# Kernel tuning notes

Hardware: AMD Instinct MI355X
Metric: run time of the kernel (lower is better)

## Reference

```python
import jax, jax.numpy as jnp
import numpy as np

INPUT, HIDDEN, CLASSES = 28, 128, 10

def setup_inputs() -> dict:
    key = jax.random.key(0)
    ks = jax.random.split(key, 8)
    B = 16384
    s_ih = 1.0 / np.sqrt(HIDDEN)
    return {
        "x": jax.random.normal(ks[0], (B, 1, 28, 28), dtype=jnp.float32),
        "W_ih": jax.random.uniform(ks[1], (HIDDEN, INPUT), jnp.float32, -s_ih, s_ih),
        "W_hh": jax.random.uniform(ks[2], (HIDDEN, HIDDEN), jnp.float32, -s_ih, s_ih),
        "b_ih": jax.random.uniform(ks[3], (HIDDEN,), jnp.float32, -s_ih, s_ih),
        "b_hh": jax.random.uniform(ks[4], (HIDDEN,), jnp.float32, -s_ih, s_ih),
        "W_fc": jax.random.uniform(ks[5], (CLASSES, HIDDEN), jnp.float32, -s_ih, s_ih),
        "b_fc": jax.random.uniform(ks[6], (CLASSES,), jnp.float32, -s_ih, s_ih),
    }

def reference(x, W_ih, W_hh, b_ih, b_hh, W_fc, b_fc):
    # x: [B,1,28,28] -> squeeze channel -> [B,T=28,I=28]
    xs = jnp.squeeze(x, axis=1)
    B = xs.shape[0]
    # precompute input projections for all timesteps: [B,T,H]
    xproj = jnp.einsum("bti,hi->bth", xs, W_ih) + b_ih + b_hh
    xproj_t = jnp.transpose(xproj, (1, 0, 2))  # [T,B,H]

    def step(h, xp):
        h_new = jnp.tanh(xp + h @ W_hh.T)
        return h_new, None

    h0 = jnp.zeros((B, HIDDEN), dtype=xs.dtype)
    h_last, _ = jax.lax.scan(step, h0, xproj_t)
    return h_last @ W_fc.T + b_fc  # [B, num_classes]
```

## Files before the change

### kernel.cpp

```cpp
#include <hip/hip_runtime.h>
#include <hip/hip_bf16.h>
#include <stdint.h>


typedef __attribute__((ext_vector_type(8))) short short8;
typedef __attribute__((ext_vector_type(4))) float f32x4;

union Frag { short8 s; uint32_t u[4]; };

#define MFMA16(a,b,c) __builtin_amdgcn_mfma_f32_16x16x32_bf16((a),(b),(c),0,0,0)

__device__ __forceinline__ uint32_t pk2(float a, float b){
    union { __hip_bfloat162 h; uint32_t u; } cv;
    cv.h = __float22bfloat162_rn(make_float2(a,b));
    return cv.u;
}
__device__ __forceinline__ float lo16f(uint32_t u){ return __builtin_bit_cast(float, u<<16); }
__device__ __forceinline__ float hi16f(uint32_t u){ return __builtin_bit_cast(float, u & 0xffff0000u); }

__device__ __forceinline__ void cvt8(const f32x4& a, const f32x4& b, Frag& hi, Frag& lo){
    float v[8];
    #pragma unroll
    for(int i=0;i<4;i++){ v[i]=a[i]; v[4+i]=b[i]; }
    #pragma unroll
    for(int q=0;q<4;q++){
        uint32_t h = pk2(v[2*q], v[2*q+1]);
        hi.u[q] = h;
        lo.u[q] = pk2(v[2*q]-lo16f(h), v[2*q+1]-hi16f(h));
    }
}

__device__ __forceinline__ int piperm(int p){
    int jt = p>>4, c = p&15;
    return 32*(jt>>1) + 8*(c>>2) + 4*(jt&1) + (c&3);
}

__device__ __forceinline__ float fast_tanh(float x){
    x = fminf(fmaxf(x, -30.f), 30.f);
    float e = __expf(2.f*x);
    return (e-1.f)*__builtin_amdgcn_rcpf(e+1.f);
}

__global__ __launch_bounds__(64,1) void rnn_fused(
    const float* __restrict__ x,   const float* __restrict__ Wih,
    const float* __restrict__ Whh, const float* __restrict__ bih,
    const float* __restrict__ bhh, const float* __restrict__ Wfc,
    const float* __restrict__ bfc, float* __restrict__ out)
{
    const int lane = threadIdx.x & 63;
    const int g = lane>>4, c = lane&15;
    const int b0 = blockIdx.x*16;
    const f32x4 zero4 = {0.f,0.f,0.f,0.f};

    Frag whh_h[8][4], whh_l[8][4];
    #pragma unroll
    for(int jt=0;jt<8;jt++){
        const int row = piperm(16*jt + c);
        const float* rp = Whh + row*128;
        #pragma unroll
        for(int kt=0;kt<4;kt++){
            f32x4 a = *(const f32x4*)(rp + kt*32 + 8*g);
            f32x4 b = *(const f32x4*)(rp + kt*32 + 8*g + 4);
            cvt8(a, b, whh_h[jt][kt], whh_l[jt][kt]);
        }
    }

    Frag wih_h[8], wih_l[8];
    {
        const int i1 = 8*g;
        const int i2 = (g<3) ? (8*g+4) : 24;
        #pragma unroll
        for(int jt=0;jt<8;jt++){
            const int row = piperm(16*jt + c);
            const float* rp = Wih + row*28;
            f32x4 a = *(const f32x4*)(rp + i1);
            f32x4 b = *(const f32x4*)(rp + i2);
            if (g==3) b = zero4;
            cvt8(a, b, wih_h[jt], wih_l[jt]);
        }
    }

    f32x4 biasr[8];
    #pragma unroll
    for(int jt=0;jt<8;jt++){
        #pragma unroll
        for(int r=0;r<4;r++){
            int q = piperm(16*jt + 4*g + r);
            biasr[jt][r] = bih[q] + bhh[q];
        }
    }

    Frag bh_h[4], bh_l[4];
    #pragma unroll
    for(int kt=0;kt<4;kt++){
        #pragma unroll
        for(int q=0;q<4;q++){ bh_h[kt].u[q]=0; bh_l[kt].u[q]=0; }
    }

    const float* xrow = x + (size_t)(b0 + c)*784;
    const int o1 = 8*g;
    const int o2 = (g<3) ? (8*g+4) : 24;

    f32x4 xA = *(const f32x4*)(xrow + o1);
    f32x4 xB = *(const f32x4*)(xrow + o2);

    for(int t=0; t<28; ++t){
        f32x4 xA_n = xA, xB_n = xB;
        if (t < 27){
            xA_n = *(const f32x4*)(xrow + (t+1)*28 + o1);
            xB_n = *(const f32x4*)(xrow + (t+1)*28 + o2);
        }
        Frag bx_h, bx_l;
        {
            f32x4 b = xB;
            if (g==3) b = zero4;
            cvt8(xA, b, bx_h, bx_l);
        }
        f32x4 acc[8];
        #pragma unroll
        for(int jt=0;jt<8;jt++){
            acc[jt] = MFMA16(wih_h[jt].s, bx_h.s, biasr[jt]);
            acc[jt] = MFMA16(wih_l[jt].s, bx_h.s, acc[jt]);
            acc[jt] = MFMA16(wih_h[jt].s, bx_l.s, acc[jt]);
            #pragma unroll
            for(int kt=0;kt<4;kt++){
                acc[jt] = MFMA16(whh_h[jt][kt].s, bh_h[kt].s, acc[jt]);
                acc[jt] = MFMA16(whh_l[jt][kt].s, bh_h[kt].s, acc[jt]);
                acc[jt] = MFMA16(whh_h[jt][kt].s, bh_l[kt].s, acc[jt]);
            }
        }
        Frag nh_h[4], nh_l[4];
        #pragma unroll
        for(int jt=0;jt<8;jt++){
            float h0 = fast_tanh(acc[jt][0]);
            float h1 = fast_tanh(acc[jt][1]);
            float h2 = fast_tanh(acc[jt][2]);
            float h3 = fast_tanh(acc[jt][3]);
            const int kt = jt>>1, q0 = (jt&1)*2;
            uint32_t u0 = pk2(h0,h1), u1 = pk2(h2,h3);
            nh_h[kt].u[q0]   = u0;
            nh_h[kt].u[q0+1] = u1;
            nh_l[kt].u[q0]   = pk2(h0-lo16f(u0), h1-hi16f(u0));
            nh_l[kt].u[q0+1] = pk2(h2-lo16f(u1), h3-hi16f(u1));
        }
        #pragma unroll
        for(int kt=0;kt<4;kt++){ bh_h[kt]=nh_h[kt]; bh_l[kt]=nh_l[kt]; }
        xA = xA_n; xB = xB_n;
    }

    Frag wfc_h[4], wfc_l[4];
    {
        const bool valid = (c < 10);
        const float* rp = Wfc + (valid ? c : 0)*128;
        #pragma unroll
        for(int kt=0;kt<4;kt++){
            f32x4 a = *(const f32x4*)(rp + kt*32 + 8*g);
            f32x4 b = *(const f32x4*)(rp + kt*32 + 8*g + 4);
            if(!valid){ a = zero4; b = zero4; }
            cvt8(a, b, wfc_h[kt], wfc_l[kt]);
        }
    }
    f32x4 accf = {0.f,0.f,0.f,0.f};
    #pragma unroll
    for(int kt=0;kt<4;kt++){
        accf = MFMA16(wfc_h[kt].s, bh_h[kt].s, accf);
        accf = MFMA16(wfc_l[kt].s, bh_h[kt].s, accf);
        accf = MFMA16(wfc_h[kt].s, bh_l[kt].s, accf);
    }
    #pragma unroll
    for(int r=0;r<4;r++){
        int cls = 4*g + r;
        if (cls < 10){
            out[(size_t)(b0+c)*10 + cls] = accf[r] + bfc[cls];
        }
    }
}

extern "C" void kernel_launch(void* const* d_in, const int* in_sizes, int n_in,
                              void* d_out, int out_size, void* d_ws, size_t ws_size,
                              hipStream_t stream)
{
    const float* x   = (const float*)d_in[0];
    const float* Wih = (const float*)d_in[1];
    const float* Whh = (const float*)d_in[2];
    const float* bih = (const float*)d_in[3];
    const float* bhh = (const float*)d_in[4];
    const float* Wfc = (const float*)d_in[5];
    const float* bfc = (const float*)d_in[6];
    float* out = (float*)d_out;

    const int nb = in_sizes[0] / 784;
    dim3 grid(nb/16), blk(64);
    hipLaunchKernelGGL(rnn_fused, grid, blk, 0, stream,
                       x, Wih, Whh, bih, bhh, Wfc, bfc, out);
}
```

Before: 163.6 us.

## Split hidden units across four waves with LDS exchange of hidden state

Each block now uses four wavefronts instead of one. Each wave owns two of the eight hidden-row tiles and keeps only its share of W_hh/W_ih in registers. The new hidden state is exchanged every timestep through double-buffered shared memory and a block barrier. The MFMA chain is also split into two independent accumulators to shorten the dependency chain. This cuts per-wave register pressure and serial MFMA latency per step, at the cost of a __syncthreads and LDS traffic on every timestep.

```diff
diff --git a/kernel.cpp b/kernel.cpp
--- a/kernel.cpp
+++ b/kernel.cpp
@@ -5,8 +5,9 @@
 
 typedef __attribute__((ext_vector_type(8))) short short8;
 typedef __attribute__((ext_vector_type(4))) float f32x4;
-
-union Frag { short8 s; uint32_t u[4]; };
+typedef __attribute__((ext_vector_type(4))) uint32_t u32x4;
+
+union Frag { short8 s; uint32_t u[4]; u32x4 v; };
 
 #define MFMA16(a,b,c) __builtin_amdgcn_mfma_f32_16x16x32_bf16((a),(b),(c),0,0,0)
 
@@ -41,52 +42,56 @@
     return (e-1.f)*__builtin_amdgcn_rcpf(e+1.f);
 }
 
-__global__ __launch_bounds__(64,1) void rnn_fused(
+__global__ __launch_bounds__(256,2) void rnn_fused4(
     const float* __restrict__ x,   const float* __restrict__ Wih,
     const float* __restrict__ Whh, const float* __restrict__ bih,
     const float* __restrict__ bhh, const float* __restrict__ Wfc,
     const float* __restrict__ bfc, float* __restrict__ out)
 {
-    const int lane = threadIdx.x & 63;
+    const int tid  = threadIdx.x;
+    const int w    = tid >> 6;
+    const int lane = tid & 63;
     const int g = lane>>4, c = lane&15;
     const int b0 = blockIdx.x*16;
     const f32x4 zero4 = {0.f,0.f,0.f,0.f};
 
-    Frag whh_h[8][4], whh_l[8][4];
-    #pragma unroll
-    for(int jt=0;jt<8;jt++){
-        const int row = piperm(16*jt + c);
+    __shared__ uint32_t lds[2][2][4][64][4];
+
+    Frag whh_h[2][4], whh_l[2][4];
+    #pragma unroll
+    for(int j=0;j<2;j++){
+        const int row = piperm(16*(2*w+j) + c);
         const float* rp = Whh + row*128;
         #pragma unroll
         for(int kt=0;kt<4;kt++){
             f32x4 a = *(const f32x4*)(rp + kt*32 + 8*g);
             f32x4 b = *(const f32x4*)(rp + kt*32 + 8*g + 4);
-            cvt8(a, b, whh_h[jt][kt], whh_l[jt][kt]);
-        }
-    }
-
-    Frag wih_h[8], wih_l[8];
+            cvt8(a, b, whh_h[j][kt], whh_l[j][kt]);
+        }
+    }
+
+    Frag wih_h[2], wih_l[2];
     {
         const int i1 = 8*g;
         const int i2 = (g<3) ? (8*g+4) : 24;
         #pragma unroll
-        for(int jt=0;jt<8;jt++){
-            const int row = piperm(16*jt + c);
+        for(int j=0;j<2;j++){
+            const int row = piperm(16*(2*w+j) + c);
             const float* rp = Wih + row*28;
             f32x4 a = *(const f32x4*)(rp + i1);
             f32x4 b = *(const f32x4*)(rp + i2);
             if (g==3) b = zero4;
-            cvt8(a, b, wih_h[jt], wih_l[jt]);
-        }
-    }
-
-    f32x4 biasr[8];
-    #pragma unroll
-    for(int jt=0;jt<8;jt++){
+            cvt8(a, b, wih_h[j], wih_l[j]);
+        }
+    }
+
+    f32x4 biasr[2];
+    #pragma unroll
+    for(int j=0;j<2;j++){
         #pragma unroll
         for(int r=0;r<4;r++){
-            int q = piperm(16*jt + 4*g + r);
-            biasr[jt][r] = bih[q] + bhh[q];
+            int q = piperm(16*(2*w+j) + 4*g + r);
+            biasr[j][r] = bih[q] + bhh[q];
         }
     }
 
@@ -116,40 +121,54 @@
             if (g==3) b = zero4;
             cvt8(xA, b, bx_h, bx_l);
         }
-        f32x4 acc[8];
-        #pragma unroll
-        for(int jt=0;jt<8;jt++){
-            acc[jt] = MFMA16(wih_h[jt].s, bx_h.s, biasr[jt]);
-            acc[jt] = MFMA16(wih_l[jt].s, bx_h.s, acc[jt]);
-            acc[jt] = MFMA16(wih_h[jt].s, bx_l.s, acc[jt]);
-            #pragma unroll
-            for(int kt=0;kt<4;kt++){
-                acc[jt] = MFMA16(whh_h[jt][kt].s, bh_h[kt].s, acc[jt]);
-                acc[jt] = MFMA16(whh_l[jt][kt].s, bh_h[kt].s, acc[jt]);
-                acc[jt] = MFMA16(whh_h[jt][kt].s, bh_l[kt].s, acc[jt]);
-            }
-        }
-        Frag nh_h[4], nh_l[4];
-        #pragma unroll
-        for(int jt=0;jt<8;jt++){
-            float h0 = fast_tanh(acc[jt][0]);
-            float h1 = fast_tanh(acc[jt][1]);
-            float h2 = fast_tanh(acc[jt][2]);
-            float h3 = fast_tanh(acc[jt][3]);
-            const int kt = jt>>1, q0 = (jt&1)*2;
+        f32x4 acc[2];
+        #pragma unroll
+        for(int j=0;j<2;j++){
+            f32x4 a1 = MFMA16(wih_h[j].s, bx_h.s, biasr[j]);
+            a1 = MFMA16(wih_l[j].s, bx_h.s, a1);
+            a1 = MFMA16(wih_h[j].s, bx_l.s, a1);
+            a1 = MFMA16(whh_h[j][0].s, bh_h[0].s, a1);
+            a1 = MFMA16(whh_l[j][0].s, bh_h[0].s, a1);
+            a1 = MFMA16(whh_h[j][0].s, bh_l[0].s, a1);
+            a1 = MFMA16(whh_h[j][1].s, bh_h[1].s, a1);
+            a1 = MFMA16(whh_l[j][1].s, bh_h[1].s, a1);
+            a1 = MFMA16(whh_h[j][1].s, bh_l[1].s, a1);
+            f32x4 a2 = MFMA16(whh_h[j][2].s, bh_h[2].s, zero4);
+            a2 = MFMA16(whh_l[j][2].s, bh_h[2].s, a2);
+            a2 = MFMA16(whh_h[j][2].s, bh_l[2].s, a2);
+            a2 = MFMA16(whh_h[j][3].s, bh_h[3].s, a2);
+            a2 = MFMA16(whh_l[j][3].s, bh_h[3].s, a2);
+            a2 = MFMA16(whh_h[j][3].s, bh_l[3].s, a2);
+            acc[j] = a1 + a2;
+        }
+        Frag nh_h, nh_l;
+        #pragma unroll
+        for(int j=0;j<2;j++){
+            float h0 = fast_tanh(acc[j][0]);
+            float h1 = fast_tanh(acc[j][1]);
+            float h2 = fast_tanh(acc[j][2]);
+            float h3 = fast_tanh(acc[j][3]);
+            const int q0 = j*2;
             uint32_t u0 = pk2(h0,h1), u1 = pk2(h2,h3);
-            nh_h[kt].u[q0]   = u0;
-            nh_h[kt].u[q0+1] = u1;
-            nh_l[kt].u[q0]   = pk2(h0-lo16f(u0), h1-hi16f(u0));
-            nh_l[kt].u[q0+1] = pk2(h2-lo16f(u1), h3-hi16f(u1));
-        }
-        #pragma unroll
-        for(int kt=0;kt<4;kt++){ bh_h[kt]=nh_h[kt]; bh_l[kt]=nh_l[kt]; }
+            nh_h.u[q0]   = u0;
+            nh_h.u[q0+1] = u1;
+            nh_l.u[q0]   = pk2(h0-lo16f(u0), h1-hi16f(u0));
+            nh_l.u[q0+1] = pk2(h2-lo16f(u1), h3-hi16f(u1));
+        }
+        const int buf = t & 1;
+        *(u32x4*)(&lds[buf][0][w][lane][0]) = nh_h.v;
+        *(u32x4*)(&lds[buf][1][w][lane][0]) = nh_l.v;
+        __syncthreads();
+        #pragma unroll
+        for(int kt=0;kt<4;kt++){
+            bh_h[kt].v = *(const u32x4*)(&lds[buf][0][kt][lane][0]);
+            bh_l[kt].v = *(const u32x4*)(&lds[buf][1][kt][lane][0]);
+        }
         xA = xA_n; xB = xB_n;
     }
 
-    Frag wfc_h[4], wfc_l[4];
-    {
+    if (w == 0){
+        Frag wfc_h[4], wfc_l[4];
         const bool valid = (c < 10);
         const float* rp = Wfc + (valid ? c : 0)*128;
         #pragma unroll
@@ -159,19 +178,19 @@
             if(!valid){ a = zero4; b = zero4; }
             cvt8(a, b, wfc_h[kt], wfc_l[kt]);
         }
-    }
-    f32x4 accf = {0.f,0.f,0.f,0.f};
-    #pragma unroll
-    for(int kt=0;kt<4;kt++){
-        accf = MFMA16(wfc_h[kt].s, bh_h[kt].s, accf);
-        accf = MFMA16(wfc_l[kt].s, bh_h[kt].s, accf);
-        accf = MFMA16(wfc_h[kt].s, bh_l[kt].s, accf);
-    }
-    #pragma unroll
-    for(int r=0;r<4;r++){
-        int cls = 4*g + r;
-        if (cls < 10){
-            out[(size_t)(b0+c)*10 + cls] = accf[r] + bfc[cls];
+        f32x4 accf = {0.f,0.f,0.f,0.f};
+        #pragma unroll
+        for(int kt=0;kt<4;kt++){
+            accf = MFMA16(wfc_h[kt].s, bh_h[kt].s, accf);
+            accf = MFMA16(wfc_l[kt].s, bh_h[kt].s, accf);
+            accf = MFMA16(wfc_h[kt].s, bh_l[kt].s, accf);
+        }
+        #pragma unroll
+        for(int r=0;r<4;r++){
+            int cls = 4*g + r;
+            if (cls < 10){
+                out[(size_t)(b0+c)*10 + cls] = accf[r] + bfc[cls];
+            }
         }
     }
 }
@@ -190,7 +209,7 @@
     float* out = (float*)d_out;
 
     const int nb = in_sizes[0] / 784;
-    dim3 grid(nb/16), blk(64);
-    hipLaunchKernelGGL(rnn_fused, grid, blk, 0, stream,
+    dim3 grid(nb/16), blk(256);
+    hipLaunchKernelGGL(rnn_fused4, grid, blk, 0, stream,
                        x, Wih, Whh, bih, bhh, Wfc, bfc, out);
 }
```

After: 148.6 us. 1.1x faster.
